# Kernel tuning notes

Hardware: AMD Instinct MI355X
Metric: run time of the kernel (lower is better)

The kernel has to match this reference:

```python
import jax, jax.numpy as jnp
import numpy as np

B, S, D, H, FF = 4, 2048, 1024, 16, 4096
DT, TARGET, ITERS = 0.1, 0.0, 5


def _ln(x, w, b):
    mu = jnp.mean(x, axis=-1, keepdims=True)
    var = jnp.mean((x - mu) ** 2, axis=-1, keepdims=True)
    return (x - mu) * jax.lax.rsqrt(var + 1e-5) * w + b


def setup_inputs() -> dict:
    key = jax.random.key(0)
    ks = iter(jax.random.split(key, 16))
    w = lambda shape: jax.random.normal(next(ks), shape, dtype=jnp.float32) * 0.02
    return {
        "x": jax.random.normal(next(ks), (B, S, D), dtype=jnp.float32),
        "ln_attn_w": jnp.ones((D,), jnp.float32), "ln_attn_b": jnp.zeros((D,), jnp.float32),
        "attn_in_w": w((3 * D, D)), "attn_in_b": jnp.zeros((3 * D,), jnp.float32),
        "attn_out_w": w((D, D)), "attn_out_b": jnp.zeros((D,), jnp.float32),
        "ln1_w": jnp.ones((D,), jnp.float32), "ln1_b": jnp.zeros((D,), jnp.float32),
        "ln2_w": jnp.ones((D,), jnp.float32), "ln2_b": jnp.zeros((D,), jnp.float32),
        "inl_u_w": w((D, D)), "inl_u_b": jnp.zeros((D,), jnp.float32),
        "inl_a_w": w((D, D)), "inl_a_b": jnp.zeros((D,), jnp.float32),
        "inl_b_w": w((D, D)), "inl_b_b": jnp.zeros((D,), jnp.float32),
        "inl_g_w": w((D, D)), "inl_g_b": jnp.zeros((D,), jnp.float32),
        "ff1_w": w((FF, D)), "ff1_b": jnp.zeros((FF,), jnp.float32),
        "ff2_w": w((D, FF)), "ff2_b": jnp.zeros((D,), jnp.float32),
    }


def reference(x, ln_attn_w, ln_attn_b, attn_in_w, attn_in_b, attn_out_w, attn_out_b,
              ln1_w, ln1_b, ln2_w, ln2_b,
              inl_u_w, inl_u_b, inl_a_w, inl_a_b, inl_b_w, inl_b_b, inl_g_w, inl_g_b,
              ff1_w, ff1_b, ff2_w, ff2_b):
    dh = D // H
    scale = 1.0 / np.sqrt(dh).astype(np.float32)
    # --- causal multi-head attention (dropout = identity, eval mode) ---
    xn = _ln(x, ln_attn_w, ln_attn_b)
    qkv = xn @ attn_in_w.T + attn_in_b            # [B,S,3D]
    q, k, v = jnp.split(qkv, 3, axis=-1)
    hsplit = lambda t: t.reshape(B, S, H, dh).transpose(0, 2, 1, 3)  # [B,H,S,dh]
    q, k, v = hsplit(q), hsplit(k), hsplit(v)
    scores = jnp.einsum('bhqd,bhkd->bhqk', q, k) * scale
    causal = jnp.triu(jnp.ones((S, S), dtype=bool), 1)
    scores = jnp.where(causal, jnp.finfo(scores.dtype).min, scores)
    probs = jax.nn.softmax(scores, axis=-1)
    attn_out = jnp.einsum('bhqk,bhkd->bhqd', probs, v).transpose(0, 2, 1, 3).reshape(B, S, D)
    attn_out = attn_out @ attn_out_w.T + attn_out_b
    x = x + attn_out
    context = attn_out
    # --- INL integrator dynamics (controllers depend only on context) ---
    xs = _ln(x, ln1_w, ln1_b)
    vs = jnp.zeros_like(xs)
    u = context @ inl_u_w.T + inl_u_b
    alpha = jax.nn.sigmoid(context @ inl_a_w.T + inl_a_b)
    beta = jax.nn.softplus(context @ inl_b_w.T + inl_b_b)
    g = jax.nn.sigmoid(context @ inl_g_w.T + inl_g_b)
    for _ in range(ITERS):
        vs = vs + DT * (alpha * (TARGET - xs) - beta * vs + u)
        xs = xs + DT * g * vs
    x = x + xs
    # --- feed-forward (exact GELU as torch default) ---
    h = _ln(x, ln2_w, ln2_b)
    x = x + (jax.nn.gelu(h @ ff1_w.T + ff1_b, approximate=False) @ ff2_w.T + ff2_b)
    return x
```

## Files before the change

kernel.cpp:

```cpp
#include <hip/hip_runtime.h>
#include <cstdint>
#include <cmath>

typedef __attribute__((ext_vector_type(4))) float floatx4;
typedef __attribute__((ext_vector_type(8))) __bf16 bf16x8;
typedef __attribute__((ext_vector_type(4))) unsigned short ushort4v;

#define DEVI static __device__ __forceinline__

DEVI unsigned short f2b(float f) {
    unsigned x = __float_as_uint(f);
    return (unsigned short)((x + 0x7fffu + ((x >> 16) & 1u)) >> 16);
}
DEVI float b2f(unsigned short u) { return __uint_as_float(((unsigned)u) << 16); }

DEVI void load16(void* lds, const void* g) {
    __builtin_amdgcn_global_load_lds(
        (__attribute__((address_space(1))) void*)(const_cast<void*>(g)),
        (__attribute__((address_space(3))) void*)lds, 16, 0, 0);
}

__global__ __launch_bounds__(256) void cvt_kernel(const float* __restrict__ src,
                                                  unsigned short* __restrict__ dst, int n4) {
    int i = blockIdx.x * 256 + threadIdx.x;
    if (i >= n4) return;
    floatx4 v = ((const floatx4*)src)[i];
    ushort4v o;
    o[0] = f2b(v[0]); o[1] = f2b(v[1]); o[2] = f2b(v[2]); o[3] = f2b(v[3]);
    ((ushort4v*)dst)[i] = o;
}

__global__ __launch_bounds__(256) void catbias_kernel(const float* __restrict__ a,
                                                      const float* __restrict__ b,
                                                      const float* __restrict__ c,
                                                      const float* __restrict__ d,
                                                      float* __restrict__ o) {
    int i = blockIdx.x * 256 + threadIdx.x;
    int p = i >> 10, j = i & 1023;
    float v = (p == 0) ? a[j] : (p == 1) ? b[j] : (p == 2) ? c[j] : d[j];
    o[i] = v;
}

__global__ __launch_bounds__(256) void ln_kernel(const float* __restrict__ in,
                                                 const float* __restrict__ w,
                                                 const float* __restrict__ b,
                                                 unsigned short* __restrict__ obf,
                                                 float* __restrict__ of) {
    const int row = blockIdx.x, tid = threadIdx.x;
    const floatx4* pr = (const floatx4*)(in + (size_t)row * 1024);
    floatx4 v = pr[tid];
    float s  = v[0] + v[1] + v[2] + v[3];
    float ss = v[0]*v[0] + v[1]*v[1] + v[2]*v[2] + v[3]*v[3];
    #pragma unroll
    for (int o = 32; o >= 1; o >>= 1) { s += __shfl_xor(s, o); ss += __shfl_xor(ss, o); }
    __shared__ float red[8];
    int wv = tid >> 6, lane = tid & 63;
    if (lane == 0) { red[wv] = s; red[4 + wv] = ss; }
    __syncthreads();
    s  = red[0] + red[1] + red[2] + red[3];
    ss = red[4] + red[5] + red[6] + red[7];
    float mu  = s * (1.0f / 1024.0f);
    float var = ss * (1.0f / 1024.0f) - mu * mu;
    float rstd = rsqrtf(var + 1e-5f);
    floatx4 wv4 = ((const floatx4*)w)[tid];
    floatx4 bv4 = ((const floatx4*)b)[tid];
    floatx4 o;
    #pragma unroll
    for (int c = 0; c < 4; c++) o[c] = (v[c] - mu) * rstd * wv4[c] + bv4[c];
    if (obf) {
        ushort4v t;
        t[0] = f2b(o[0]); t[1] = f2b(o[1]); t[2] = f2b(o[2]); t[3] = f2b(o[3]);
        ((ushort4v*)(obf + (size_t)row * 1024))[tid] = t;
    }
    if (of) ((floatx4*)(of + (size_t)row * 1024))[tid] = o;
}

__global__ __launch_bounds__(256) void integrator_kernel(const float* __restrict__ xs0,
                                                         const unsigned short* __restrict__ uabg,
                                                         float* __restrict__ xio) {
    size_t i = (size_t)blockIdx.x * 256 + threadIdx.x;
    size_t tok = i >> 8;
    int grp = (int)(i & 255) * 4;
    const unsigned short* ubase = uabg + tok * 4096 + grp;
    ushort4v uu = *(const ushort4v*)(ubase);
    ushort4v aa = *(const ushort4v*)(ubase + 1024);
    ushort4v bb = *(const ushort4v*)(ubase + 2048);
    ushort4v gg = *(const ushort4v*)(ubase + 3072);
    floatx4 xsv = ((const floatx4*)xs0)[i];
    floatx4 x1  = ((const floatx4*)xio)[i];
    floatx4 res;
    #pragma unroll
    for (int c = 0; c < 4; c++) {
        float u = b2f(uu[c]), a = b2f(aa[c]), bt = b2f(bb[c]), g = b2f(gg[c]);
        float xs = xsv[c], vs = 0.f;
        #pragma unroll
        for (int t = 0; t < 5; t++) {
            vs += 0.1f * (-a * xs - bt * vs + u);
            xs += 0.1f * g * vs;
        }
        res[c] = x1[c] + xs;
    }
    ((floatx4*)xio)[i] = res;
}

template <int EPI>
__global__ __launch_bounds__(256) void gemm_bt(const unsigned short* __restrict__ A,
                                               const unsigned short* __restrict__ W,
                                               const float* __restrict__ bias, int K,
                                               unsigned short* __restrict__ ob0,
                                               unsigned short* __restrict__ ob1,
                                               unsigned short* __restrict__ ob2,
                                               float* __restrict__ of0,
                                               const float* __restrict__ xres) {
    __shared__ unsigned short sA[128 * 32];
    __shared__ unsigned short sB[128 * 32];
    const int tid = threadIdx.x;
    const int wave = tid >> 6, lane = tid & 63;
    const int ln = lane & 15, quad = lane >> 4;
    const size_t m0 = (size_t)blockIdx.y * 128;
    const int n0 = blockIdx.x * 128;
    const int wm = (wave >> 1) * 64, wn = (wave & 1) * 64;

    const floatx4 z4 = {0.f, 0.f, 0.f, 0.f};
    floatx4 acc[4][4];
    #pragma unroll
    for (int mt = 0; mt < 4; mt++)
        #pragma unroll
        for (int nt = 0; nt < 4; nt++) acc[mt][nt] = z4;

    const int arow = wave * 16 + (lane >> 2);
    const int acol = (lane & 3) * 8;
    const unsigned short* gA = A + (m0 + (size_t)arow) * K + acol;
    const unsigned short* gB = W + ((size_t)(n0 + arow)) * K + acol;
    const size_t rs64 = (size_t)64 * K;
    unsigned short* lA0 = &sA[wave * 512];
    unsigned short* lA1 = &sA[(wave + 4) * 512];
    unsigned short* lB0 = &sB[wave * 512];
    unsigned short* lB1 = &sB[(wave + 4) * 512];

    for (int k0 = 0; k0 < K; k0 += 32) {
        load16(lA0, gA + k0);
        load16(lA1, gA + rs64 + k0);
        load16(lB0, gB + k0);
        load16(lB1, gB + rs64 + k0);
        __syncthreads();
        bf16x8 af[4], bfr[4];
        #pragma unroll
        for (int mt = 0; mt < 4; mt++)
            af[mt] = *(const bf16x8*)&sA[(wm + mt * 16 + ln) * 32 + quad * 8];
        #pragma unroll
        for (int nt = 0; nt < 4; nt++)
            bfr[nt] = *(const bf16x8*)&sB[(wn + nt * 16 + ln) * 32 + quad * 8];
        #pragma unroll
        for (int mt = 0; mt < 4; mt++)
            #pragma unroll
            for (int nt = 0; nt < 4; nt++)
                acc[mt][nt] = __builtin_amdgcn_mfma_f32_16x16x32_bf16(af[mt], bfr[nt], acc[mt][nt], 0, 0, 0);
        __syncthreads();
    }

    const size_t rowb = m0 + wm + quad * 4;
    const int colb = n0 + wn + ln;
    #pragma unroll
    for (int mt = 0; mt < 4; mt++) {
        #pragma unroll
        for (int nt = 0; nt < 4; nt++) {
            const int n = colb + nt * 16;
            const float bs = bias[n];
            #pragma unroll
            for (int r = 0; r < 4; r++) {
                const size_t row = rowb + mt * 16 + r;
                float c = acc[mt][nt][r] + bs;
                if constexpr (EPI == 0) {
                    int sect = n >> 10, d1 = n & 1023, h = d1 >> 6, d = d1 & 63;
                    int bb = (int)(row >> 11), s = (int)(row & 2047);
                    size_t bh = (size_t)(bb * 16 + h);
                    if (sect == 0)      ob0[(bh * 2048 + s) * 64 + d] = f2b(c);
                    else if (sect == 1) ob1[(bh * 2048 + s) * 64 + d] = f2b(c);
                    else                ob2[(bh * 64 + d) * 2048 + s] = f2b(c);
                } else if constexpr (EPI == 1) {
                    size_t idx = row * 1024 + n;
                    ob0[idx] = f2b(c);
                    of0[idx] = xres[idx] + c;
                } else if constexpr (EPI == 2) {
                    int p = n >> 10;
                    float v;
                    if (p == 0)       v = c;
                    else if (p == 2)  v = fmaxf(c, 0.f) + log1pf(__expf(-fabsf(c)));
                    else              v = 1.f / (1.f + __expf(-c));
                    ob0[row * 4096 + n] = f2b(v);
                } else if constexpr (EPI == 3) {
                    float v = 0.5f * c * (1.f + erff(c * 0.70710678118654752f));
                    ob0[row * 4096 + n] = f2b(v);
                } else {
                    size_t idx = row * 1024 + n;
                    of0[idx] += c;
                }
            }
        }
    }
}

#define PSTR 72
__global__ __launch_bounds__(256, 3) void attn_kernel(const unsigned short* __restrict__ Qb,
                                                      const unsigned short* __restrict__ Kb,
                                                      const unsigned short* __restrict__ Vtb,
                                                      unsigned short* __restrict__ Ob) {
    __shared__ unsigned short sK[2][64 * 64];
    __shared__ unsigned short sVt[2][64 * 64];
    __shared__ unsigned short sQP[128 * PSTR];
    const int pr = blockIdx.x;
    const int bh = blockIdx.y;
    const int tid = threadIdx.x, wave = tid >> 6, lane = tid & 63;
    const int ln = lane & 15, quad = lane >> 4;
    const unsigned short* Q  = Qb  + (size_t)bh * 2048 * 64;
    const unsigned short* Kp = Kb  + (size_t)bh * 2048 * 64;
    const unsigned short* Vt = Vtb + (size_t)bh * 64 * 2048;

    const int rl  = lane >> 3;
    const int gsw = (((lane & 7) ^ rl)) * 8;
    const int sseg = wave * 2;
    const unsigned short* kbase = Kp + (size_t)(sseg * 8 + rl) * 64 + gsw;
    const unsigned short* vbase = Vt + (size_t)(sseg * 8 + rl) * 2048 + gsw;
    unsigned short* sP = &sQP[wave * 32 * PSTR];
    const int bb = bh >> 4, h = bh & 15;
    const floatx4 z4 = {0.f, 0.f, 0.f, 0.f};

    #pragma unroll 1
    for (int phase = 0; phase < 2; phase++) {
        const int qt = phase ? pr : (15 - pr);
        const int q0 = qt * 128;
        const int T = 2 * qt + 2;

        #pragma unroll
        for (int i = 0; i < 4; i++) {
            int s = wave * 4 + i;
            load16(&sQP[s * 512], Q + (size_t)(q0 + s * 8 + rl) * 64 + gsw);
        }
        load16(&sK[0][sseg * 512], kbase);
        load16(&sK[0][(sseg + 1) * 512], kbase + (size_t)8 * 64);
        load16(&sVt[0][sseg * 512], vbase);
        load16(&sVt[0][(sseg + 1) * 512], vbase + (size_t)8 * 2048);
        asm volatile("s_waitcnt vmcnt(0)" ::: "memory");
        asm volatile("s_barrier" ::: "memory");

        bf16x8 aq[2][2];
        #pragma unroll
        for (int mt = 0; mt < 2; mt++)
            #pragma unroll
            for (int ks = 0; ks < 2; ks++)
                aq[mt][ks] = *(const bf16x8*)&sQP[(wave * 32 + mt * 16 + ln) * 64 +
                                                  (((ks * 4 + quad) ^ (ln & 7)) * 8)];
        asm volatile("s_waitcnt lgkmcnt(0)" ::: "memory");
        asm volatile("s_barrier" ::: "memory");

        floatx4 Oacc[2][4];
        float m_run[2][4], l_run[2][4];
        #pragma unroll
        for (int mt = 0; mt < 2; mt++)
            #pragma unroll
            for (int j = 0; j < 4; j++) { Oacc[mt][j] = z4; m_run[mt][j] = -1e30f; l_run[mt][j] = 0.f; }

        const int wave_first = q0 + wave * 32;
        const int wave_last  = wave_first + 31;

        #pragma unroll 1
        for (int t = 0; t < T; t++) {
            const int kk0 = t * 64;
            const int cur = t & 1;
            if (t + 1 < T) {
                const unsigned short* kg = kbase + (size_t)(kk0 + 64) * 64;
                const unsigned short* vg = vbase + (size_t)(kk0 + 64);
                load16(&sK[cur ^ 1][sseg * 512], kg);
                load16(&sK[cur ^ 1][(sseg + 1) * 512], kg + (size_t)8 * 64);
                load16(&sVt[cur ^ 1][sseg * 512], vg);
                load16(&sVt[cur ^ 1][(sseg + 1) * 512], vg + (size_t)8 * 2048);
                asm volatile("s_waitcnt vmcnt(4)" ::: "memory");
            } else {
                asm volatile("s_waitcnt vmcnt(0)" ::: "memory");
            }
            asm volatile("s_barrier" ::: "memory");

            if (kk0 <= wave_last) {
                floatx4 Sc[2][4];
                #pragma unroll
                for (int mt = 0; mt < 2; mt++)
                    #pragma unroll
                    for (int nt = 0; nt < 4; nt++) Sc[mt][nt] = z4;
                #pragma unroll
                for (int ks = 0; ks < 2; ks++) {
                    #pragma unroll
                    for (int nt = 0; nt < 4; nt++) {
                        bf16x8 bk = *(const bf16x8*)&sK[cur][(nt * 16 + ln) * 64 +
                                                             (((ks * 4 + quad) ^ (ln & 7)) * 8)];
                        #pragma unroll
                        for (int mt = 0; mt < 2; mt++)
                            Sc[mt][nt] = __builtin_amdgcn_mfma_f32_16x16x32_bf16(aq[mt][ks], bk, Sc[mt][nt], 0, 0, 0);
                    }
                }
                const bool diag = (kk0 + 63 > wave_first);
                #pragma unroll
                for (int mt = 0; mt < 2; mt++)
                    #pragma unroll
                    for (int nt = 0; nt < 4; nt++)
                        #pragma unroll
                        for (int r = 0; r < 4; r++) {
                            float v = Sc[mt][nt][r] * 0.125f;
                            if (diag) {
                                int rowg = wave_first + mt * 16 + quad * 4 + r;
                                int colg = kk0 + nt * 16 + ln;
                                if (colg > rowg) v = -1e30f;
                            }
                            Sc[mt][nt][r] = v;
                        }
                float alpha[2][4];
                #pragma unroll
                for (int mt = 0; mt < 2; mt++)
                    #pragma unroll
                    for (int r = 0; r < 4; r++) {
                        float mx = fmaxf(fmaxf(Sc[mt][0][r], Sc[mt][1][r]), fmaxf(Sc[mt][2][r], Sc[mt][3][r]));
                        #pragma unroll
                        for (int off = 1; off < 16; off <<= 1) mx = fmaxf(mx, __shfl_xor(mx, off));
                        float mnew = fmaxf(m_run[mt][r], mx);
                        alpha[mt][r] = __expf(m_run[mt][r] - mnew);
                        m_run[mt][r] = mnew;
                    }
                #pragma unroll
                for (int mt = 0; mt < 2; mt++)
                    #pragma unroll
                    for (int r = 0; r < 4; r++) {
                        float rs = 0.f;
                        #pragma unroll
                        for (int nt = 0; nt < 4; nt++) {
                            float p = __expf(Sc[mt][nt][r] - m_run[mt][r]);
                            Sc[mt][nt][r] = p;
                            rs += p;
                        }
                        #pragma unroll
                        for (int off = 1; off < 16; off <<= 1) rs += __shfl_xor(rs, off);
                        l_run[mt][r] = l_run[mt][r] * alpha[mt][r] + rs;
                    }
                #pragma unroll
                for (int mt = 0; mt < 2; mt++)
                    #pragma unroll
                    for (int nt = 0; nt < 4; nt++)
                        #pragma unroll
                        for (int r = 0; r < 4; r++) Oacc[mt][nt][r] *= alpha[mt][r];
                #pragma unroll
                for (int mt = 0; mt < 2; mt++)
                    #pragma unroll
                    for (int nt = 0; nt < 4; nt++)
                        #pragma unroll
                        for (int r = 0; r < 4; r++)
                            sP[(mt * 16 + quad * 4 + r) * PSTR + nt * 16 + ln] = f2b(Sc[mt][nt][r]);
                #pragma unroll
                for (int kp = 0; kp < 2; kp++) {
                    bf16x8 ap[2];
                    #pragma unroll
                    for (int mt = 0; mt < 2; mt++)
                        ap[mt] = *(const bf16x8*)&sP[(mt * 16 + ln) * PSTR + kp * 32 + quad * 8];
                    #pragma unroll
                    for (int nt = 0; nt < 4; nt++) {
                        bf16x8 bv = *(const bf16x8*)&sVt[cur][(nt * 16 + ln) * 64 +
                                                              (((kp * 4 + quad) ^ (ln & 7)) * 8)];
                        #pragma unroll
                        for (int mt = 0; mt < 2; mt++)
                            Oacc[mt][nt] = __builtin_amdgcn_mfma_f32_16x16x32_bf16(ap[mt], bv, Oacc[mt][nt], 0, 0, 0);
                    }
                }
            }
            asm volatile("s_barrier" ::: "memory");
        }

        #pragma unroll
        for (int mt = 0; mt < 2; mt++)
            #pragma unroll
            for (int nt = 0; nt < 4; nt++)
                #pragma unroll
                for (int r = 0; r < 4; r++) {
                    float o = Oacc[mt][nt][r] / l_run[mt][r];
                    int srow = q0 + wave * 32 + mt * 16 + quad * 4 + r;
                    size_t tok = (size_t)bb * 2048 + srow;
                    Ob[tok * 1024 + h * 64 + nt * 16 + ln] = f2b(o);
                }
    }
}

extern "C" void kernel_launch(void* const* d_in, const int* in_sizes, int n_in,
                              void* d_out, int out_size, void* d_ws, size_t ws_size,
                              hipStream_t stream) {
    const float* x          = (const float*)d_in[0];
    const float* ln_attn_w  = (const float*)d_in[1];
    const float* ln_attn_b  = (const float*)d_in[2];
    const float* attn_in_w  = (const float*)d_in[3];
    const float* attn_in_b  = (const float*)d_in[4];
    const float* attn_out_w = (const float*)d_in[5];
    const float* attn_out_b = (const float*)d_in[6];
    const float* ln1_w      = (const float*)d_in[7];
    const float* ln1_b      = (const float*)d_in[8];
    const float* ln2_w      = (const float*)d_in[9];
    const float* ln2_b      = (const float*)d_in[10];
    const float* inl_u_w    = (const float*)d_in[11];
    const float* inl_u_b    = (const float*)d_in[12];
    const float* inl_a_w    = (const float*)d_in[13];
    const float* inl_a_b    = (const float*)d_in[14];
    const float* inl_b_w    = (const float*)d_in[15];
    const float* inl_b_b    = (const float*)d_in[16];
    const float* inl_g_w    = (const float*)d_in[17];
    const float* inl_g_b    = (const float*)d_in[18];
    const float* ff1_w      = (const float*)d_in[19];
    const float* ff1_b      = (const float*)d_in[20];
    const float* ff2_w      = (const float*)d_in[21];
    const float* ff2_b      = (const float*)d_in[22];
    float* out = (float*)d_out;

    char* ws = (char*)d_ws;
    unsigned short* Wqkv  = (unsigned short*)(ws);
    unsigned short* Wout  = (unsigned short*)(ws + 6291456);
    unsigned short* Winl  = (unsigned short*)(ws + 8388608);
    unsigned short* Wff1  = (unsigned short*)(ws + 16777216);
    unsigned short* Wff2  = (unsigned short*)(ws + 25165824);
    unsigned short* xnb   = (unsigned short*)(ws + 33554432);
    unsigned short* qb    = (unsigned short*)(ws + 50331648);
    unsigned short* kb    = (unsigned short*)(ws + 67108864);
    unsigned short* vtb   = (unsigned short*)(ws + 83886080);
    unsigned short* attnb = (unsigned short*)(ws + 100663296);
    unsigned short* ctxb  = (unsigned short*)(ws + 117440512);
    float*          xs    = (float*)(ws + 134217728);
    float*          bias4 = (float*)(ws + 167772160);
    unsigned short* uabg  = (unsigned short*)(ws + 50331648);
    unsigned short* ff1b  = (unsigned short*)(ws + 50331648);

    cvt_kernel<<<3072, 256, 0, stream>>>(attn_in_w, Wqkv, 786432);
    cvt_kernel<<<1024, 256, 0, stream>>>(attn_out_w, Wout, 262144);
    cvt_kernel<<<1024, 256, 0, stream>>>(inl_u_w, Winl + 0, 262144);
    cvt_kernel<<<1024, 256, 0, stream>>>(inl_a_w, Winl + 1048576, 262144);
    cvt_kernel<<<1024, 256, 0, stream>>>(inl_b_w, Winl + 2097152, 262144);
    cvt_kernel<<<1024, 256, 0, stream>>>(inl_g_w, Winl + 3145728, 262144);
    cvt_kernel<<<4096, 256, 0, stream>>>(ff1_w, Wff1, 1048576);
    cvt_kernel<<<4096, 256, 0, stream>>>(ff2_w, Wff2, 1048576);
    catbias_kernel<<<16, 256, 0, stream>>>(inl_u_b, inl_a_b, inl_b_b, inl_g_b, bias4);

    ln_kernel<<<8192, 256, 0, stream>>>(x, ln_attn_w, ln_attn_b, xnb, nullptr);
    gemm_bt<0><<<dim3(24, 64), 256, 0, stream>>>(xnb, Wqkv, attn_in_b, 1024, qb, kb, vtb, nullptr, nullptr);
    attn_kernel<<<dim3(8, 64), 256, 0, stream>>>(qb, kb, vtb, attnb);
    gemm_bt<1><<<dim3(8, 64), 256, 0, stream>>>(attnb, Wout, attn_out_b, 1024, ctxb, nullptr, nullptr, out, x);
    ln_kernel<<<8192, 256, 0, stream>>>(out, ln1_w, ln1_b, nullptr, xs);
    gemm_bt<2><<<dim3(32, 64), 256, 0, stream>>>(ctxb, Winl, bias4, 1024, uabg, nullptr, nullptr, nullptr, nullptr);
    integrator_kernel<<<8192, 256, 0, stream>>>(xs, uabg, out);
    ln_kernel<<<8192, 256, 0, stream>>>(out, ln2_w, ln2_b, xnb, nullptr);
    gemm_bt<3><<<dim3(32, 64), 256, 0, stream>>>(xnb, Wff1, ff1_b, 1024, ff1b, nullptr, nullptr, nullptr, nullptr);
    gemm_bt<4><<<dim3(8, 64), 256, 0, stream>>>(ff1b, Wff2, ff2_b, 4096, nullptr, nullptr, nullptr, out, nullptr);
}
```

Baseline: 915.3 us.

## Double-buffer GEMM LDS tiles with async prefetch and XOR swizzle

Shared-memory tiles in the bf16 GEMM become double-buffered. The next K-slice is fetched with global_load_lds while MFMAs run on the current one, using manual vmcnt waits and barriers in place of two full __syncthreads per step. The global column offset is also XOR-swizzled, with a matching swizzled LDS read index, to reduce LDS bank conflicts on fragment loads. LDS use doubles, which may lower occupancy, and the hand-written waitcnt logic is fragile.

```diff
diff --git a/kernel.cpp b/kernel.cpp
--- a/kernel.cpp
+++ b/kernel.cpp
@@ -112,8 +112,8 @@
                                                unsigned short* __restrict__ ob2,
                                                float* __restrict__ of0,
                                                const float* __restrict__ xres) {
-    __shared__ unsigned short sA[128 * 32];
-    __shared__ unsigned short sB[128 * 32];
+    __shared__ unsigned short sA[2][128 * 32];
+    __shared__ unsigned short sB[2][128 * 32];
     const int tid = threadIdx.x;
     const int wave = tid >> 6, lane = tid & 63;
     const int ln = lane & 15, quad = lane >> 4;
@@ -128,35 +128,52 @@
         #pragma unroll
         for (int nt = 0; nt < 4; nt++) acc[mt][nt] = z4;
 
-    const int arow = wave * 16 + (lane >> 2);
-    const int acol = (lane & 3) * 8;
-    const unsigned short* gA = A + (m0 + (size_t)arow) * K + acol;
-    const unsigned short* gB = W + ((size_t)(n0 + arow)) * K + acol;
+    const int r16 = lane >> 2;
+    const int gsw = ((lane & 3) ^ (r16 & 3)) * 8;
+    const int arow = wave * 16 + r16;
+    const unsigned short* gA = A + (m0 + (size_t)arow) * K + gsw;
+    const unsigned short* gB = W + ((size_t)(n0 + arow)) * K + gsw;
     const size_t rs64 = (size_t)64 * K;
-    unsigned short* lA0 = &sA[wave * 512];
-    unsigned short* lA1 = &sA[(wave + 4) * 512];
-    unsigned short* lB0 = &sB[wave * 512];
-    unsigned short* lB1 = &sB[(wave + 4) * 512];
-
-    for (int k0 = 0; k0 < K; k0 += 32) {
-        load16(lA0, gA + k0);
-        load16(lA1, gA + rs64 + k0);
-        load16(lB0, gB + k0);
-        load16(lB1, gB + rs64 + k0);
-        __syncthreads();
+    const int so = wave * 512;
+
+    load16(&sA[0][so], gA);
+    load16(&sA[0][so + 2048], gA + rs64);
+    load16(&sB[0][so], gB);
+    load16(&sB[0][so + 2048], gB + rs64);
+
+    const int T = K >> 5;
+    const int swr = (quad ^ (ln & 3)) * 8;
+
+    #pragma unroll 1
+    for (int t = 0; t < T; t++) {
+        const int cur = t & 1;
+        if (t + 1 < T) {
+            const int k = (t + 1) * 32;
+            load16(&sA[cur ^ 1][so], gA + k);
+            load16(&sA[cur ^ 1][so + 2048], gA + rs64 + k);
+            load16(&sB[cur ^ 1][so], gB + k);
+            load16(&sB[cur ^ 1][so + 2048], gB + rs64 + k);
+            asm volatile("s_waitcnt vmcnt(4)" ::: "memory");
+        } else {
+            asm volatile("s_waitcnt vmcnt(0)" ::: "memory");
+        }
+        asm volatile("s_barrier" ::: "memory");
+
         bf16x8 af[4], bfr[4];
         #pragma unroll
         for (int mt = 0; mt < 4; mt++)
-            af[mt] = *(const bf16x8*)&sA[(wm + mt * 16 + ln) * 32 + quad * 8];
+            af[mt] = *(const bf16x8*)&sA[cur][(wm + mt * 16 + ln) * 32 + swr];
         #pragma unroll
         for (int nt = 0; nt < 4; nt++)
-            bfr[nt] = *(const bf16x8*)&sB[(wn + nt * 16 + ln) * 32 + quad * 8];
+            bfr[nt] = *(const bf16x8*)&sB[cur][(wn + nt * 16 + ln) * 32 + swr];
         #pragma unroll
         for (int mt = 0; mt < 4; mt++)
             #pragma unroll
             for (int nt = 0; nt < 4; nt++)
                 acc[mt][nt] = __builtin_amdgcn_mfma_f32_16x16x32_bf16(af[mt], bfr[nt], acc[mt][nt], 0, 0, 0);
-        __syncthreads();
+
+        asm volatile("s_waitcnt lgkmcnt(0)" ::: "memory");
+        asm volatile("s_barrier" ::: "memory");
     }
 
     const size_t rowb = m0 + wm + quad * 4;
```

Measured after the change: 890.3 us. 1.03x faster.

## Load GEMM fragments directly from global into registers with double buffering

Applied to the files above, without the earlier changes.

Drops the LDS staging and block barriers from the bf16 GEMM main loop. Each wave now loads its MFMA operand fragments straight from global memory into registers, ping-ponging two register sets so the next k-step's loads overlap the current MFMAs. This removes __syncthreads and LDS traffic, but tiles shared between waves are now fetched twice from global/L2 with less coalesced 16-byte row-strided accesses. It also raises register pressure and assumes K/32 is even.

```diff
diff --git a/kernel.cpp b/kernel.cpp
--- a/kernel.cpp
+++ b/kernel.cpp
@@ -112,8 +112,6 @@
                                                unsigned short* __restrict__ ob2,
                                                float* __restrict__ of0,
                                                const float* __restrict__ xres) {
-    __shared__ unsigned short sA[128 * 32];
-    __shared__ unsigned short sB[128 * 32];
     const int tid = threadIdx.x;
     const int wave = tid >> 6, lane = tid & 63;
     const int ln = lane & 15, quad = lane >> 4;
@@ -128,35 +126,42 @@
         #pragma unroll
         for (int nt = 0; nt < 4; nt++) acc[mt][nt] = z4;
 
-    const int arow = wave * 16 + (lane >> 2);
-    const int acol = (lane & 3) * 8;
-    const unsigned short* gA = A + (m0 + (size_t)arow) * K + acol;
-    const unsigned short* gB = W + ((size_t)(n0 + arow)) * K + acol;
-    const size_t rs64 = (size_t)64 * K;
-    unsigned short* lA0 = &sA[wave * 512];
-    unsigned short* lA1 = &sA[(wave + 4) * 512];
-    unsigned short* lB0 = &sB[wave * 512];
-    unsigned short* lB1 = &sB[(wave + 4) * 512];
-
-    for (int k0 = 0; k0 < K; k0 += 32) {
-        load16(lA0, gA + k0);
-        load16(lA1, gA + rs64 + k0);
-        load16(lB0, gB + k0);
-        load16(lB1, gB + rs64 + k0);
-        __syncthreads();
-        bf16x8 af[4], bfr[4];
+    const unsigned short* pa = A + (m0 + wm + ln) * (size_t)K + quad * 8;
+    const unsigned short* pb = W + ((size_t)(n0 + wn + ln)) * K + quad * 8;
+    const size_t ts = (size_t)16 * K;
+
+    const int T = K >> 5;
+
+    bf16x8 fa0[4], fb0[4], fa1[4], fb1[4];
+    #pragma unroll
+    for (int mt = 0; mt < 4; mt++) fa0[mt] = *(const bf16x8*)(pa + mt * ts);
+    #pragma unroll
+    for (int nt = 0; nt < 4; nt++) fb0[nt] = *(const bf16x8*)(pb + nt * ts);
+
+    #pragma unroll 1
+    for (int t = 0; t < T; t += 2) {
+        const int k1 = (t + 1) << 5;
+        #pragma unroll
+        for (int mt = 0; mt < 4; mt++) fa1[mt] = *(const bf16x8*)(pa + mt * ts + k1);
+        #pragma unroll
+        for (int nt = 0; nt < 4; nt++) fb1[nt] = *(const bf16x8*)(pb + nt * ts + k1);
         #pragma unroll
         for (int mt = 0; mt < 4; mt++)
-            af[mt] = *(const bf16x8*)&sA[(wm + mt * 16 + ln) * 32 + quad * 8];
-        #pragma unroll
-        for (int nt = 0; nt < 4; nt++)
-            bfr[nt] = *(const bf16x8*)&sB[(wn + nt * 16 + ln) * 32 + quad * 8];
+            #pragma unroll
+            for (int nt = 0; nt < 4; nt++)
+                acc[mt][nt] = __builtin_amdgcn_mfma_f32_16x16x32_bf16(fa0[mt], fb0[nt], acc[mt][nt], 0, 0, 0);
+        if (t + 2 < T) {
+            const int k2 = (t + 2) << 5;
+            #pragma unroll
+            for (int mt = 0; mt < 4; mt++) fa0[mt] = *(const bf16x8*)(pa + mt * ts + k2);
+            #pragma unroll
+            for (int nt = 0; nt < 4; nt++) fb0[nt] = *(const bf16x8*)(pb + nt * ts + k2);
+        }
         #pragma unroll
         for (int mt = 0; mt < 4; mt++)
             #pragma unroll
             for (int nt = 0; nt < 4; nt++)
-                acc[mt][nt] = __builtin_amdgcn_mfma_f32_16x16x32_bf16(af[mt], bfr[nt], acc[mt][nt], 0, 0, 0);
-        __syncthreads();
+                acc[mt][nt] = __builtin_amdgcn_mfma_f32_16x16x32_bf16(fa1[mt], fb1[nt], acc[mt][nt], 0, 0, 0);
     }
 
     const size_t rowb = m0 + wm + quad * 4;
```

New measurement: 1.445 ms. 57.8% more time.
